# Optimization experiments

Hardware: AMD Instinct MI355X
Metric: run time of the kernel (lower is better)

The kernel has to match this reference:

```python
import jax, jax.numpy as jnp
import numpy as np

# ---- config (matches init_kwargs + VMamba/MambaIR SS2D defaults) ----
B, LEN, C, H, W = 2, 3, 64, 64, 64
N_STATE = 16           # d_state
D_INNER = 2 * C        # expand=2
DT_RANK = C // 16      # ceil(d_model/16)
K = 4                  # 4 scan directions
EPS = 1e-5


def _ln_last(x, g, b):
    m = x.mean(-1, keepdims=True)
    v = x.var(-1, keepdims=True)
    return (x - m) * jax.lax.rsqrt(v + EPS) * g + b


def _instance_ln(x):
    # kalman.utils.layer_norm: normalize each sample over (C,H,W), no affine
    m = x.mean(axis=(1, 2, 3), keepdims=True)
    v = x.var(axis=(1, 2, 3), keepdims=True)
    return (x - m) * jax.lax.rsqrt(v + EPS)


def _gn(x, g, b):
    # GroupNorm with num_groups=1 on NCHW
    m = x.mean(axis=(1, 2, 3), keepdims=True)
    v = x.var(axis=(1, 2, 3), keepdims=True)
    return (x - m) * jax.lax.rsqrt(v + EPS) * g[None, :, None, None] + b[None, :, None, None]


def _conv2d(x, w, b, groups=1):
    y = jax.lax.conv_general_dilated(x, w, (1, 1), 'SAME',
            dimension_numbers=('NCHW', 'OIHW', 'NCHW'), feature_group_count=groups)
    return y + b[None, :, None, None]


def _selective_scan(xs, dts, Bs, Cs, A, Ds, dt_bias):
    # xs, dts: (Bt,K,D,L); Bs, Cs: (Bt,K,N,L); A: (K,D,N); Ds, dt_bias: (K,D)
    delta = jax.nn.softplus(dts + dt_bias[None, :, :, None])
    u_t = jnp.moveaxis(xs, -1, 0)      # (L,Bt,K,D)
    d_t = jnp.moveaxis(delta, -1, 0)
    B_t = jnp.moveaxis(Bs, -1, 0)      # (L,Bt,K,N)
    C_t = jnp.moveaxis(Cs, -1, 0)
    h0 = jnp.zeros((xs.shape[0], K, xs.shape[2], A.shape[-1]), xs.dtype)

    def step(h, inp):
        u, d, Bv, Cv = inp
        dA = jnp.exp(d[..., None] * A)                                  # (Bt,K,D,N)
        h = dA * h + d[..., None] * Bv[:, :, None, :] * u[..., None]
        y = jnp.einsum('bkdn,bkn->bkd', h, Cv)
        return h, y

    _, ys = jax.lax.scan(step, h0, (u_t, d_t, B_t, C_t))
    ys = jnp.moveaxis(ys, 0, -1)                                        # (Bt,K,D,L)
    return ys + xs * Ds[None, :, :, None]


def _ss2d(x, in_proj_w, dwconv_w, dwconv_b, x_proj_w, dt_proj_w, dt_proj_b,
          A_logs, Ds, out_norm_g, out_norm_b, out_proj_w):
    Bt, Hh, Ww, Cc = x.shape
    L = Hh * Ww
    xz = x @ in_proj_w.T                               # (Bt,H,W,2*Di)
    xx, z = jnp.split(xz, 2, axis=-1)
    xx = jnp.transpose(xx, (0, 3, 1, 2))               # (Bt,Di,H,W)
    xx = jax.nn.silu(_conv2d(xx, dwconv_w, dwconv_b, groups=D_INNER))
    hw = xx.reshape(Bt, D_INNER, L)
    wh = jnp.transpose(xx, (0, 1, 3, 2)).reshape(Bt, D_INNER, L)
    xs = jnp.stack([hw, wh, hw[..., ::-1], wh[..., ::-1]], axis=1)      # (Bt,4,Di,L)
    x_dbl = jnp.einsum('bkdl,kcd->bkcl', xs, x_proj_w)
    dts = jnp.einsum('bkrl,kdr->bkdl', x_dbl[:, :, :DT_RANK], dt_proj_w)
    Bs = x_dbl[:, :, DT_RANK:DT_RANK + N_STATE]
    Cs = x_dbl[:, :, DT_RANK + N_STATE:]
    A = -jnp.exp(A_logs)                               # (K,Di,N)
    out_y = _selective_scan(xs, dts, Bs, Cs, A, Ds, dt_proj_b)
    inv = out_y[:, 2:4, :, ::-1]

    def wh2hw(y):
        return jnp.transpose(y.reshape(Bt, D_INNER, Ww, Hh), (0, 1, 3, 2)).reshape(Bt, D_INNER, L)

    y = out_y[:, 0] + inv[:, 0] + wh2hw(out_y[:, 1]) + wh2hw(inv[:, 1])
    y = jnp.transpose(y.reshape(Bt, D_INNER, Hh, Ww), (0, 2, 3, 1))
    y = _ln_last(y, out_norm_g, out_norm_b)
    y = y * jax.nn.silu(z)
    return y @ out_proj_w.T


def setup_inputs() -> dict:
    key = jax.random.key(0)
    ks = jax.random.split(key, 16)
    rn = lambda k, s, sc=0.05: jax.random.normal(k, s, jnp.float32) * sc
    inp = {}
    inp['image_sequence'] = jax.random.normal(ks[0], (B, LEN, C, H, W), jnp.float32)
    inp['difficult_zone'] = jax.random.normal(ks[1], (B, C, H, W), jnp.float32)
    inp['sigma'] = jax.random.uniform(ks[2], (B, C, H, W), jnp.float32)
    inp['gn1_g'] = jnp.ones((3 * C,)); inp['gn1_b'] = jnp.zeros((3 * C,))
    inp['conv1_w'] = rn(ks[3], (C, 3 * C, 3, 3)); inp['conv1_b'] = jnp.zeros((C,))
    inp['gn2_g'] = jnp.ones((C,)); inp['gn2_b'] = jnp.zeros((C,))
    inp['conv2_w'] = rn(ks[4], (C, C, 3, 3)); inp['conv2_b'] = jnp.zeros((C,))
    inp['skip_w'] = rn(ks[5], (C, 3 * C, 1, 1)); inp['skip_b'] = jnp.zeros((C,))
    inp['ln1_g'] = jnp.ones((C,)); inp['ln1_b'] = jnp.zeros((C,))
    inp['ln2_g'] = jnp.ones((C,)); inp['ln2_b'] = jnp.zeros((C,))
    inp['in_proj_w'] = rn(ks[6], (2 * D_INNER, C))
    inp['dwconv_w'] = rn(ks[7], (D_INNER, 1, 3, 3)); inp['dwconv_b'] = jnp.zeros((D_INNER,))
    inp['x_proj_w'] = rn(ks[8], (K, DT_RANK + 2 * N_STATE, D_INNER))
    inp['dt_proj_w'] = rn(ks[9], (K, D_INNER, DT_RANK), 0.2)
    inp['dt_proj_b'] = rn(ks[10], (K, D_INNER), 0.1)
    inp['A_logs'] = jnp.log(jnp.broadcast_to(jnp.arange(1, N_STATE + 1, dtype=jnp.float32), (K, D_INNER, N_STATE)))
    inp['Ds'] = jnp.ones((K, D_INNER))
    inp['out_norm_g'] = jnp.ones((D_INNER,)); inp['out_norm_b'] = jnp.zeros((D_INNER,))
    inp['out_proj_w'] = rn(ks[11], (C, D_INNER))
    inp['fc1_w'] = rn(ks[12], (C, C)); inp['fc1_b'] = jnp.zeros((C,))
    inp['fc2_w'] = rn(ks[13], (C, C)); inp['fc2_b'] = jnp.zeros((C,))
    return inp


def reference(image_sequence, difficult_zone, sigma,
              gn1_g, gn1_b, conv1_w, conv1_b, gn2_g, gn2_b, conv2_w, conv2_b, skip_w, skip_b,
              ln1_g, ln1_b, ln2_g, ln2_b,
              in_proj_w, dwconv_w, dwconv_b, x_proj_w, dt_proj_w, dt_proj_b,
              A_logs, Ds, out_norm_g, out_norm_b, out_proj_w,
              fc1_w, fc1_b, fc2_w, fc2_b):
    Bsz, Lf, Cc, Hh, Ww = image_sequence.shape
    # per-frame layer_norm; frames are independent so fold them into batch
    img = _instance_ln(image_sequence.reshape(Bsz * Lf, Cc, Hh, Ww)).reshape(Bsz, Lf, Cc, Hh, Ww)
    dz = jnp.broadcast_to(difficult_zone[:, None], (Bsz, Lf, Cc, Hh, Ww))
    sg = jnp.broadcast_to(sigma[:, None], (Bsz, Lf, Cc, Hh, Ww))
    x = jnp.concatenate([dz, img, sg], axis=2).reshape(Bsz * Lf, 3 * Cc, Hh, Ww)
    # ConvolutionalResBlock (GN -> SiLU -> conv, x2, + 1x1 skip)
    h = _conv2d(jax.nn.silu(_gn(x, gn1_g, gn1_b)), conv1_w, conv1_b)
    h = _conv2d(jax.nn.silu(_gn(h, gn2_g, gn2_b)), conv2_w, conv2_b)
    x = h + _conv2d(x, skip_w, skip_b)
    # VSSBlock (pre-norm): x + SS2D(LN(x)); x + Mlp(LN(x))
    x = jnp.transpose(x, (0, 2, 3, 1))                 # NHWC
    x = x + _ss2d(_ln_last(x, ln1_g, ln1_b), in_proj_w, dwconv_w, dwconv_b,
                  x_proj_w, dt_proj_w, dt_proj_b, A_logs, Ds,
                  out_norm_g, out_norm_b, out_proj_w)
    xm = _ln_last(x, ln2_g, ln2_b)
    x = x + (jax.nn.gelu(xm @ fc1_w.T + fc1_b) @ fc2_w.T + fc2_b)
    x = jnp.transpose(x, (0, 3, 1, 2)).reshape(Bsz, Lf, Cc, Hh, Ww)
    return x
```

## Files before the change

kernel.cpp:

```cpp
#include <hip/hip_runtime.h>
#include <hip/hip_bf16.h>

typedef unsigned short ushortT;
typedef short short8v __attribute__((ext_vector_type(8)));
typedef float float4v __attribute__((ext_vector_type(4)));

#define NBL 6
#define NC 64
#define NC3 192
#define NHW 4096
#define NDI 128
#define NNS 16
#define NDR 4
#define NK 4
#define NL 4096
#define NCH 128
#define SCLEN 32
#define NSTATE 49152
#define NSAMP 262144

static const size_t F_XCAT  = 0;
static const size_t F_ACT1  = 4718592;
static const size_t F_H1    = 9437184;
static const size_t F_ACT2  = 11010048;
static const size_t F_H2    = 12582912;
static const size_t F_XRES  = 14155776;
static const size_t F_XXIN  = 15728640;
static const size_t F_Z     = 18874368;
static const size_t F_XXC   = 22020096;
static const size_t F_XDBL  = 25165824;
static const size_t F_YS    = 28704768;
static const size_t F_WTS   = 41287680;
static const size_t F_X1    = 44433408;
static const size_t F_X2    = 46006272;
static const size_t F_STATS = 47579136;
static const size_t F_TOTAL = 47579184;

__device__ __forceinline__ float wred64(float v) {
#pragma unroll
  for (int m = 32; m; m >>= 1) v += __shfl_xor(v, m, 64);
  return v;
}

__device__ __forceinline__ float silu(float v) {
  return v / (1.f + __expf(-v));
}

__device__ __forceinline__ ushortT f2bf(float f) {
  unsigned int u = __builtin_bit_cast(unsigned int, f);
  unsigned int r = (u + 0x7FFFu + ((u >> 16) & 1u)) >> 16;
  return (ushortT)r;
}

__device__ __forceinline__ float bf2f(ushortT u) {
  return __builtin_bit_cast(float, (unsigned int)u << 16);
}

__device__ __forceinline__ int map_pos(int k, int l) {
  if (k == 0) return l;
  if (k == 1) return ((l & 63) << 6) | (l >> 6);
  if (k == 2) return 4095 - l;
  int lp = 4095 - l;
  return ((lp & 63) << 6) | (lp >> 6);
}

__device__ __forceinline__ float softplus_fast(float a) {
  float t = exp2f(a * 1.44269504f);
  float r = 0.69314718f * __log2f(1.f + t);
  return (a > 20.f) ? a : r;
}

__device__ __forceinline__ void pow_tree(float E1, float4v& e0, float4v& e1,
                                         float4v& e2, float4v& e3) {
  float E2 = E1 * E1, E3 = E2 * E1, E4 = E2 * E2;
  float E5 = E4 * E1, E6 = E4 * E2, E7 = E4 * E3, E8 = E4 * E4;
  e0[0] = E1; e0[1] = E2; e0[2] = E3; e0[3] = E4;
  e1[0] = E5; e1[1] = E6; e1[2] = E7; e1[3] = E8;
  e2[0] = E8 * E1; e2[1] = E8 * E2; e2[2] = E8 * E3; e2[3] = E8 * E4;
  e3[0] = E8 * E5; e3[1] = E8 * E6; e3[2] = E8 * E7; e3[3] = E8 * E8;
}

__global__ __launch_bounds__(256) void prep_kernel(const float* __restrict__ skw,
                                                   const float* __restrict__ ipw,
                                                   const float* __restrict__ opw,
                                                   const float* __restrict__ f1w,
                                                   const float* __restrict__ f2w,
                                                   const float* __restrict__ c1w,
                                                   const float* __restrict__ c2w,
                                                   float* __restrict__ wt_sk,
                                                   float* __restrict__ wt_ip,
                                                   float* __restrict__ wt_op,
                                                   float* __restrict__ wt_f1,
                                                   float* __restrict__ wt_f2,
                                                   ushortT* __restrict__ wb1,
                                                   ushortT* __restrict__ wb2) {
  int bi = blockIdx.x;
  int t = threadIdx.x;
  if (bi < 48) {
    int id = bi * 256 + t;
    int c = id / 64, o = id % 64;
    wt_sk[id] = skw[o * 192 + c];
  } else if (bi < 112) {
    int id = (bi - 48) * 256 + t;
    int c = id / 256, o = id % 256;
    wt_ip[id] = ipw[o * 64 + c];
  } else if (bi < 144) {
    int id = (bi - 112) * 256 + t;
    int c = id / 64, o = id % 64;
    wt_op[id] = opw[o * 128 + c];
  } else if (bi < 160) {
    int id = (bi - 144) * 256 + t;
    int c = id / 64, o = id % 64;
    wt_f1[id] = f1w[o * 64 + c];
  } else if (bi < 176) {
    int id = (bi - 160) * 256 + t;
    int c = id / 64, o = id % 64;
    wt_f2[id] = f2w[o * 64 + c];
  } else if (bi < 608) {
    int id = (bi - 176) * 256 + t;
    int j = id & 7, lane = (id >> 3) & 63, nt = (id >> 9) & 3;
    int rest = id >> 11;
    int kt = rest % 6, tap = rest / 6;
    int oc = nt * 16 + (lane & 15);
    int ic = kt * 32 + ((lane >> 4) << 3) + j;
    int r = tap / 3, s = tap % 3;
    wb1[id] = f2bf(c1w[(((size_t)oc * 192 + ic) * 3 + r) * 3 + s]);
  } else {
    int id = (bi - 608) * 256 + t;
    int j = id & 7, lane = (id >> 3) & 63, nt = (id >> 9) & 3;
    int rest = id >> 11;
    int kt = rest % 2, tap = rest / 2;
    int oc = nt * 16 + (lane & 15);
    int ic = kt * 32 + ((lane >> 4) << 3) + j;
    int r = tap / 3, s = tap % 3;
    wb2[id] = f2bf(c2w[(((size_t)oc * 64 + ic) * 3 + r) * 3 + s]);
  }
}

__global__ __launch_bounds__(256) void stats1_all_kernel(const float* __restrict__ img,
                                                         const float* __restrict__ dz,
                                                         const float* __restrict__ sg,
                                                         double* __restrict__ part) {
  int bi = blockIdx.x;
  int s = bi >> 5, j = bi & 31;
  const float* srcb = (s < 6) ? (img + (size_t)s * NSAMP)
                   : (s < 8) ? (dz + (size_t)(s - 6) * NSAMP)
                             : (sg + (size_t)(s - 8) * NSAMP);
  int slice = NSAMP >> 5;
  const float4* p = (const float4*)(srcb + (size_t)j * slice);
  int n4 = slice >> 2;
  double dsum = 0.0, dsq = 0.0;
  for (int i = threadIdx.x; i < n4; i += 256) {
    float4 v = p[i];
    dsum += (double)((v.x + v.y) + (v.z + v.w));
    dsq += (double)v.x * v.x + (double)v.y * v.y + (double)v.z * v.z + (double)v.w * v.w;
  }
  __shared__ double s1[256], s2[256];
  s1[threadIdx.x] = dsum; s2[threadIdx.x] = dsq;
  __syncthreads();
  for (int off = 128; off; off >>= 1) {
    if (threadIdx.x < off) { s1[threadIdx.x] += s1[threadIdx.x + off]; s2[threadIdx.x] += s2[threadIdx.x + off]; }
    __syncthreads();
  }
  if (threadIdx.x == 0) { part[2 * bi] = s1[0]; part[2 * bi + 1] = s2[0]; }
}

__global__ __launch_bounds__(256) void stats1_kernel(const float* __restrict__ in, int n,
                                                     double* __restrict__ part) {
  int bi = blockIdx.x;
  int s = bi >> 5, j = bi & 31;
  int slice = n >> 5;
  const float4* p = (const float4*)(in + (size_t)s * n + (size_t)j * slice);
  int n4 = slice >> 2;
  double dsum = 0.0, dsq = 0.0;
  for (int i = threadIdx.x; i < n4; i += 256) {
    float4 v = p[i];
    dsum += (double)((v.x + v.y) + (v.z + v.w));
    dsq += (double)v.x * v.x + (double)v.y * v.y + (double)v.z * v.z + (double)v.w * v.w;
  }
  __shared__ double s1[256], s2[256];
  s1[threadIdx.x] = dsum; s2[threadIdx.x] = dsq;
  __syncthreads();
  for (int off = 128; off; off >>= 1) {
    if (threadIdx.x < off) { s1[threadIdx.x] += s1[threadIdx.x + off]; s2[threadIdx.x] += s2[threadIdx.x + off]; }
    __syncthreads();
  }
  if (threadIdx.x == 0) { part[2 * bi] = s1[0]; part[2 * bi + 1] = s2[0]; }
}

__global__ __launch_bounds__(64) void stats2_kernel(const double* __restrict__ part, int n,
                                                    float* __restrict__ mean_out,
                                                    float* __restrict__ rstd_out) {
  int s = blockIdx.x;
  int lane = threadIdx.x;
  double sum = 0.0, sq = 0.0;
  if (lane < 32) { sum = part[2 * (s * 32 + lane)]; sq = part[2 * (s * 32 + lane) + 1]; }
#pragma unroll
  for (int m = 16; m; m >>= 1) { sum += __shfl_xor(sum, m, 64); sq += __shfl_xor(sq, m, 64); }
  if (lane == 0) {
    double mean = sum / n;
    double var = sq / n - mean * mean;
    mean_out[s] = (float)mean;
    rstd_out[s] = (float)(1.0 / sqrt(var + 1e-5));
  }
}

__global__ __launch_bounds__(64) void stats2_comb_kernel(const double* __restrict__ part,
                                                         float* __restrict__ stats) {
  int s = blockIdx.x;
  int lane = threadIdx.x;
  if (s < 6) {
    double sum = 0.0, sq = 0.0;
    if (lane < 32) { sum = part[2 * (s * 32 + lane)]; sq = part[2 * (s * 32 + lane) + 1]; }
#pragma unroll
    for (int m = 16; m; m >>= 1) { sum += __shfl_xor(sum, m, 64); sq += __shfl_xor(sq, m, 64); }
    if (lane == 0) {
      double mean = sum / NSAMP;
      double var = sq / NSAMP - mean * mean;
      stats[s] = (float)mean;
      stats[8 + s] = (float)(1.0 / sqrt(var + 1e-5));
    }
    return;
  }
  if (lane == 0) {
    double sums[10], sqs[10];
    for (int q = 0; q < 10; ++q) {
      double a = 0.0, b2 = 0.0;
      for (int j = 0; j < 32; ++j) { a += part[2 * (q * 32 + j)]; b2 += part[2 * (q * 32 + j) + 1]; }
      sums[q] = a; sqs[q] = b2;
    }
    const double N = (double)NSAMP;
    for (int bl = 0; bl < 6; ++bl) {
      int b = bl / 3;
      double mi = sums[bl] / N;
      double vi = sqs[bl] / N - mi * mi;
      double ssq_norm = N * (vi / (vi + 1e-5));
      double sum_cat = sums[6 + b] + sums[8 + b];
      double ssq_cat = sqs[6 + b] + ssq_norm + sqs[8 + b];
      double mean = sum_cat / (3.0 * N);
      double var = ssq_cat / (3.0 * N) - mean * mean;
      stats[16 + bl] = (float)mean;
      stats[24 + bl] = (float)(1.0 / sqrt(var + 1e-5));
    }
  }
}

__global__ __launch_bounds__(256) void gnsilu_cat_kernel(const float* __restrict__ img,
                                                         const float* __restrict__ dz,
                                                         const float* __restrict__ sg,
                                                         const float* __restrict__ g,
                                                         const float* __restrict__ b,
                                                         const float* __restrict__ stats,
                                                         ushortT* __restrict__ outb) {
  int bi = blockIdx.x;
  int bl = bi >> 6, h = bi & 63;
  int bb = bl / 3;
  __shared__ ushortT tile[NC3][66];
  float mi = stats[bl], rsi = stats[8 + bl];
  float mc = stats[16 + bl], rsc = stats[24 + bl];
  int t = threadIdx.x;
  for (int idx = t; idx < NC3 * 64; idx += 256) {
    int ch = idx >> 6, w = idx & 63;
    int hw = (h << 6) + w;
    float v;
    if (ch < 64) v = dz[((size_t)bb * NC + ch) * NHW + hw];
    else if (ch < 128) v = (img[((size_t)bl * NC + (ch - 64)) * NHW + hw] - mi) * rsi;
    else v = sg[((size_t)bb * NC + (ch - 128)) * NHW + hw];
    v = (v - mc) * rsc * g[ch] + b[ch];
    tile[ch][w] = f2bf(silu(v));
  }
  __syncthreads();
  constexpr int C8 = NC3 / 8;
  for (int idx = t; idx < 64 * C8; idx += 256) {
    int w = idx / C8, c8 = idx % C8;
    short8v v;
#pragma unroll
    for (int j = 0; j < 8; ++j) v[j] = (short)tile[c8 * 8 + j][w];
    *(short8v*)&outb[(size_t)(bl * 4096 + h * 64 + w) * NC3 + c8 * 8] = v;
  }
}

__global__ __launch_bounds__(256) void gnsilu_t_kernel(const float* __restrict__ in,
                                                       const float* __restrict__ g,
                                                       const float* __restrict__ b,
                                                       const float* __restrict__ stats,
                                                       ushortT* __restrict__ outb) {
  int bi = blockIdx.x;
  int bl = bi >> 6, h = bi & 63;
  __shared__ ushortT tile[NC][66];
  float m = stats[bl], rs = stats[8 + bl];
  int t = threadIdx.x;
  for (int idx = t; idx < NC * 64; idx += 256) {
    int ch = idx >> 6, w = idx & 63;
    float v = in[(((size_t)bl * NC + ch) << 12) + (h << 6) + w];
    v = (v - m) * rs * g[ch] + b[ch];
    tile[ch][w] = f2bf(silu(v));
  }
  __syncthreads();
  constexpr int C8 = NC / 8;
  for (int idx = t; idx < 64 * C8; idx += 256) {
    int w = idx / C8, c8 = idx % C8;
    short8v v;
#pragma unroll
    for (int j = 0; j < 8; ++j) v[j] = (short)tile[c8 * 8 + j][w];
    *(short8v*)&outb[(size_t)(bl * 4096 + h * 64 + w) * NC + c8 * 8] = v;
  }
}

template <int CIN>
__global__ __launch_bounds__(256) void conv_mfma_kernel(const ushortT* __restrict__ actb,
                                                        const ushortT* __restrict__ wb,
                                                        const float* __restrict__ bias,
                                                        float* __restrict__ out) {
  constexpr int KT = CIN / 32;
  constexpr int STRIDE = CIN + 8;
  constexpr int C8 = CIN / 8;
  int bi = blockIdx.x;
  int nh = bi & 1;
  int h = (bi >> 1) & 63;
  int bl = bi >> 7;
  int t = threadIdx.x;
  int wv = t >> 6, lane = t & 63;
  __shared__ ushortT lds[66 * STRIDE];
  float4v acc0 = {0.f, 0.f, 0.f, 0.f};
  float4v acc1 = {0.f, 0.f, 0.f, 0.f};
  int lrow = lane & 15;
  int lk = (lane >> 4) << 3;
  for (int dy = 0; dy < 3; ++dy) {
    int hh = h + dy - 1;
    bool valid = (hh >= 0) && (hh < 64);
    int hc = valid ? hh : 0;
    if (dy) __syncthreads();
    const ushortT* src = actb + (size_t)(bl * 4096 + hc * 64) * CIN;
    for (int idx = t; idx < 64 * C8; idx += 256) {
      int w = idx / C8, c8 = idx % C8;
      short8v v = {0, 0, 0, 0, 0, 0, 0, 0};
      if (valid) v = *(const short8v*)&src[(size_t)w * CIN + c8 * 8];
      *(short8v*)&lds[(w + 1) * STRIDE + c8 * 8] = v;
    }
    if (t < 2 * C8) {
      int which = t / C8, c8 = t % C8;
      short8v z = {0, 0, 0, 0, 0, 0, 0, 0};
      *(short8v*)&lds[(which ? 65 : 0) * STRIDE + c8 * 8] = z;
    }
    __syncthreads();
    for (int dx = 0; dx < 3; ++dx) {
      int tap = dy * 3 + dx;
      int wl = (wv << 4) + lrow + dx;
#pragma unroll
      for (int kt = 0; kt < KT; ++kt) {
        short8v a = *(const short8v*)&lds[wl * STRIDE + kt * 32 + lk];
        const ushortT* wp = wb + ((size_t)(((tap * KT + kt) * 4 + (nh << 1)) * 64 + lane) << 3);
        short8v b0 = *(const short8v*)&wp[0];
        short8v b1 = *(const short8v*)&wp[512];
        acc0 = __builtin_amdgcn_mfma_f32_16x16x32_bf16(a, b0, acc0, 0, 0, 0);
        acc1 = __builtin_amdgcn_mfma_f32_16x16x32_bf16(a, b1, acc1, 0, 0, 0);
      }
    }
  }
  int oc0 = (nh << 5) + lrow;
  int oc1 = oc0 + 16;
  int w0 = (wv << 4) + ((lane >> 4) << 2);
  float bv0 = bias[oc0], bv1 = bias[oc1];
  float4 o0 = make_float4(acc0[0] + bv0, acc0[1] + bv0, acc0[2] + bv0, acc0[3] + bv0);
  float4 o1 = make_float4(acc1[0] + bv1, acc1[1] + bv1, acc1[2] + bv1, acc1[3] + bv1);
  *(float4*)&out[(((size_t)bl * 64 + oc0) << 12) + (h << 6) + w0] = o0;
  *(float4*)&out[(((size_t)bl * 64 + oc1) << 12) + (h << 6) + w0] = o1;
}

__global__ __launch_bounds__(256) void skip_kernel(const float* __restrict__ img,
                                                   const float* __restrict__ dz,
                                                   const float* __restrict__ sg,
                                                   const float* __restrict__ stats,
                                                   const float* __restrict__ h2,
                                                   const float* __restrict__ skwt,
                                                   const float* __restrict__ skb,
                                                   float* __restrict__ xres) {
  int bi = blockIdx.x;
  int bl = bi >> 6, h = bi & 63;
  int bb = bl / 3;
  int t = threadIdx.x;
  int oc = t & 63, w0 = (t >> 6) << 4;
  float mi = stats[bl], rsi = stats[8 + bl];
  __shared__ float lds[64][64];
  float acc[16];
#pragma unroll
  for (int i = 0; i < 16; ++i) acc[i] = 0.f;
  for (int cc = 0; cc < 3; ++cc) {
    __syncthreads();
    for (int idx = t; idx < 4096; idx += 256) {
      int ch = idx >> 6, w = idx & 63;
      int hw = (h << 6) + w;
      float v;
      if (cc == 0) v = dz[((size_t)bb * NC + ch) * NHW + hw];
      else if (cc == 1) v = (img[((size_t)bl * NC + ch) * NHW + hw] - mi) * rsi;
      else v = sg[((size_t)bb * NC + ch) * NHW + hw];
      lds[ch][w] = v;
    }
    __syncthreads();
    for (int ch = 0; ch < 64; ++ch) {
      float wv = skwt[((cc << 6) + ch) * 64 + oc];
#pragma unroll
      for (int i = 0; i < 16; ++i) acc[i] += wv * lds[ch][w0 + i];
    }
  }
  float bv = skb[oc];
  int p0 = (h << 6) + w0;
#pragma unroll
  for (int i = 0; i < 16; ++i) {
    float hv = h2[(((size_t)bl * 64 + oc) << 12) + p0 + i];
    xres[((size_t)bl * NHW + p0 + i) * 64 + oc] = acc[i] + bv + hv;
  }
}

__global__ __launch_bounds__(256) void inproj_kernel(const float* __restrict__ xres,
                                                     const float* __restrict__ g,
                                                     const float* __restrict__ b,
                                                     const float* __restrict__ wt,
                                                     float* __restrict__ xxin,
                                                     float* __restrict__ z) {
  int wv = threadIdx.x >> 6, lane = threadIdx.x & 63;
  size_t pi0 = (size_t)blockIdx.x << 4;
  __shared__ float xb[64][16];
  float gv = g[lane], bv = b[lane];
#pragma unroll
  for (int j = 0; j < 4; ++j) {
    int p = (wv << 2) + j;
    float x = xres[(pi0 + p) * 64 + lane];
    float s = wred64(x);
    float s2 = wred64(x * x);
    float m = s * (1.f / 64), var = s2 * (1.f / 64) - m * m;
    float rstd = rsqrtf(var + 1e-5f);
    xb[lane][p] = (x - m) * rstd * gv + bv;
  }
  __syncthreads();
  int oc = (wv << 6) + lane;
  float4v a0 = {0.f, 0.f, 0.f, 0.f}, a1 = a0, a2 = a0, a3 = a0;
  for (int c = 0; c < 64; ++c) {
    float w = wt[(c << 8) + oc];
    const float4v* xr = (const float4v*)&xb[c][0];
    a0 += w * xr[0];
    a1 += w * xr[1];
    a2 += w * xr[2];
    a3 += w * xr[3];
  }
  float acc[16];
  *(float4v*)&acc[0] = a0;
  *(float4v*)&acc[4] = a1;
  *(float4v*)&acc[8] = a2;
  *(float4v*)&acc[12] = a3;
  float* dst = (oc < 128) ? xxin : z;
  int oco = (oc < 128) ? oc : (oc - 128);
#pragma unroll
  for (int p = 0; p < 16; ++p) dst[((pi0 + p) << 7) + oco] = acc[p];
}

__global__ __launch_bounds__(256) void dwconv_kernel(const float* __restrict__ xx,
                                                     const float* __restrict__ w,
                                                     const float* __restrict__ b,
                                                     float* __restrict__ out) {
  size_t gid = (size_t)blockIdx.x * 256 + threadIdx.x;
  int d = gid & 127;
  size_t pi = gid >> 7;
  int p = (int)(pi & 4095);
  int bl = (int)(pi >> 12);
  int h = p >> 6, wq = p & 63;
  float acc = b[d];
  const float* wr = w + d * 9;
#pragma unroll
  for (int dy = -1; dy <= 1; ++dy) {
    int hh = h + dy;
    if (hh < 0 || hh >= 64) continue;
#pragma unroll
    for (int dx = -1; dx <= 1; ++dx) {
      int ww = wq + dx;
      if (ww < 0 || ww >= 64) continue;
      acc += wr[(dy + 1) * 3 + (dx + 1)] * xx[(((size_t)bl << 12) + (hh << 6) + ww) * 128 + d];
    }
  }
  out[pi * 128 + d] = silu(acc);
}

__global__ __launch_bounds__(256) void xdbl_kernel(const float* __restrict__ xxc,
                                                   const float* __restrict__ xpw,
                                                   float* __restrict__ xdbl) {
  int bi = blockIdx.x;
  int lt = bi & 63;
  int korder = (bi >> 6) & 1;
  int bl = bi >> 7;
  int lbase = lt << 6;
  __shared__ float xs[64 * 128];
  int t = threadIdx.x;
#pragma unroll
  for (int it = 0; it < 8; ++it) {
    int idx = it * 256 + t;
    int i = idx >> 5, d4 = idx & 31;
    int l = lbase + i;
    int pos = korder ? (((l & 63) << 6) | (l >> 6)) : l;
    float4 v = *(const float4*)&xxc[((size_t)bl * NHW + pos) * 128 + (d4 << 2)];
    int slot = d4 ^ (i & 7);
    *(float4*)&xs[i * 128 + (slot << 2)] = v;
  }
  __syncthreads();
  int wv = __builtin_amdgcn_readfirstlane(t >> 6);
  int lane = t & 63;
  int k_w = korder + ((wv >= 2) ? 2 : 0);
  int c0 = (wv & 1) * 18;
  float acc[18];
#pragma unroll
  for (int j = 0; j < 18; ++j) acc[j] = 0.f;
  const float* wbase = xpw + (size_t)(k_w * 36 + c0) * 128;
  for (int d4 = 0; d4 < 32; ++d4) {
    int slot = d4 ^ (lane & 7);
    float4 x4 = *(const float4*)&xs[lane * 128 + (slot << 2)];
#pragma unroll
    for (int j = 0; j < 18; ++j) {
      float4 w4 = *(const float4*)&wbase[j * 128 + (d4 << 2)];
      acc[j] += w4.x * x4.x + w4.y * x4.y + w4.z * x4.z + w4.w * x4.w;
    }
  }
  int lout = (k_w < 2) ? (lbase + lane) : (4095 - lbase - lane);
  size_t obase = ((size_t)(bl * 4 + k_w) * 36 + c0) * (size_t)NL + lout;
#pragma unroll
  for (int j = 0; j < 18; ++j)
    xdbl[obase + (size_t)j * NL] = acc[j];
}

__global__ __launch_bounds__(128) void scan_pass1_kernel(const float* __restrict__ xdbl,
                                                         const float* __restrict__ xxc,
                                                         const float* __restrict__ dtw,
                                                         const float* __restrict__ dtb,
                                                         const float* __restrict__ Alog,
                                                         float* __restrict__ chunkSdt,
                                                         ushortT* __restrict__ chunkH16) {
  int bi = blockIdx.x;
  int chunk = bi & (NCH - 1);
  int bk = bi >> 7;
  int k = bk & 3, bl = bk >> 2;
  int d = threadIdx.x;
  float4 wv = *(const float4*)(dtw + (size_t)(((k << 7) + d) << 2));
  float bias = dtb[(k << 7) + d];
  const float* ar = Alog + (size_t)(((k << 7) + d) << 4);
  float a1v = -__expf(ar[0]) * 1.44269504f;
  bool geom = true;
#pragma unroll
  for (int n = 1; n < 16; ++n) {
    float an = -__expf(ar[n]) * 1.44269504f;
    geom = geom && (fabsf(an - (float)(n + 1) * a1v) <= 1e-3f * fabsf((float)(n + 1) * a1v) + 1e-6f);
  }
  __shared__ float xd[SCLEN][20];
  int l0 = chunk << 5;
  for (int idx = threadIdx.x; idx < 20 * SCLEN; idx += 128) {
    int c = idx >> 5, li = idx & 31;
    xd[li][c] = xdbl[((size_t)bk * 36 + c) * (size_t)NL + l0 + li];
  }
  __syncthreads();
  const float* uB = xxc + ((size_t)bl << 19) + d;
  float4v h0 = {0.f, 0.f, 0.f, 0.f}, h1 = h0, h2 = h0, h3 = h0;
  float sdt = 0.f;
  float u_nxt = uB[(size_t)map_pos(k, l0) << 7];
  if (geom) {
#pragma unroll 2
    for (int li = 0; li < SCLEN; ++li) {
      float u = u_nxt;
      int nl = (li < SCLEN - 1) ? (li + 1) : (SCLEN - 1);
      u_nxt = uB[(size_t)map_pos(k, l0 + nl) << 7];
      const float4v* row = (const float4v*)&xd[li][0];
      float4v q0 = row[0];
      float accq = bias + wv.x * q0[0] + wv.y * q0[1] + wv.z * q0[2] + wv.w * q0[3];
      float dt = softplus_fast(accq);
      float dtu = dt * u;
      sdt += dt;
      float4v b0 = row[1], b1 = row[2], b2 = row[3], b3 = row[4];
      float4v e0, e1, e2, e3;
      pow_tree(exp2f(a1v * dt), e0, e1, e2, e3);
      h0 = e0 * h0 + dtu * b0;
      h1 = e1 * h1 + dtu * b1;
      h2 = e2 * h2 + dtu * b2;
      h3 = e3 * h3 + dtu * b3;
    }
  } else {
    float4v a0v, a1q, a2q, a3q;
#pragma unroll
    for (int j = 0; j < 4; ++j) {
      a0v[j] = -__expf(ar[j]) * 1.44269504f;
      a1q[j] = -__expf(ar[4 + j]) * 1.44269504f;
      a2q[j] = -__expf(ar[8 + j]) * 1.44269504f;
      a3q[j] = -__expf(ar[12 + j]) * 1.44269504f;
    }
    for (int li = 0; li < SCLEN; ++li) {
      float u = u_nxt;
      int nl = (li < SCLEN - 1) ? (li + 1) : (SCLEN - 1);
      u_nxt = uB[(size_t)map_pos(k, l0 + nl) << 7];
      const float4v* row = (const float4v*)&xd[li][0];
      float4v q0 = row[0];
      float accq = bias + wv.x * q0[0] + wv.y * q0[1] + wv.z * q0[2] + wv.w * q0[3];
      float dt = softplus_fast(accq);
      float dtu = dt * u;
      sdt += dt;
      float4v b0 = row[1], b1 = row[2], b2 = row[3], b3 = row[4];
      float4v e0, e1, e2, e3;
#pragma unroll
      for (int j = 0; j < 4; ++j) {
        e0[j] = exp2f(a0v[j] * dt);
        e1[j] = exp2f(a1q[j] * dt);
        e2[j] = exp2f(a2q[j] * dt);
        e3[j] = exp2f(a3q[j] * dt);
      }
      h0 = e0 * h0 + dtu * b0;
      h1 = e1 * h1 + dtu * b1;
      h2 = e2 * h2 + dtu * b2;
      h3 = e3 * h3 + dtu * b3;
    }
  }
  size_t base = (size_t)chunk * NSTATE + (((size_t)bk << 7) + (size_t)d) * 16;
  chunkSdt[(size_t)chunk * 3072 + (bk << 7) + d] = sdt;
  short8v s0, s1;
#pragma unroll
  for (int j = 0; j < 4; ++j) {
    s0[j] = (short)f2bf(h0[j]);
    s0[4 + j] = (short)f2bf(h1[j]);
    s1[j] = (short)f2bf(h2[j]);
    s1[4 + j] = (short)f2bf(h3[j]);
  }
  *(short8v*)&chunkH16[base + 0] = s0;
  *(short8v*)&chunkH16[base + 8] = s1;
}

__global__ __launch_bounds__(256) void scan_pass2_kernel(const float* __restrict__ chunkSdt,
                                                         const ushortT* __restrict__ chunkH16,
                                                         const float* __restrict__ Alog,
                                                         ushortT* __restrict__ chunkHS16) {
  size_t state = (size_t)blockIdx.x * 256 + threadIdx.x;
  float an = -__expf(Alog[state & 8191]) * 1.44269504f;
  int kd = (int)(state >> 4);
  float h = 0.f;
  for (int j = 0; j < NCH; ++j) {
    size_t idx = (size_t)j * NSTATE + state;
    chunkHS16[idx] = f2bf(h);
    float sdt = chunkSdt[(size_t)j * 3072 + kd];
    h = exp2f(an * sdt) * h + bf2f(chunkH16[idx]);
  }
}

__global__ __launch_bounds__(128) void scan_pass3_kernel(const float* __restrict__ xdbl,
                                                         const float* __restrict__ xxc,
                                                         const float* __restrict__ dtw,
                                                         const float* __restrict__ dtb,
                                                         const float* __restrict__ Alog,
                                                         const ushortT* __restrict__ chunkHS16,
                                                         ushortT* __restrict__ ys16) {
  int bi = blockIdx.x;
  int chunk = bi & (NCH - 1);
  int bk = bi >> 7;
  int k = bk & 3, bl = bk >> 2;
  int d = threadIdx.x;
  float4 wv = *(const float4*)(dtw + (size_t)(((k << 7) + d) << 2));
  float bias = dtb[(k << 7) + d];
  const float* ar = Alog + (size_t)(((k << 7) + d) << 4);
  float a1v = -__expf(ar[0]) * 1.44269504f;
  bool geom = true;
#pragma unroll
  for (int n = 1; n < 16; ++n) {
    float an = -__expf(ar[n]) * 1.44269504f;
    geom = geom && (fabsf(an - (float)(n + 1) * a1v) <= 1e-3f * fabsf((float)(n + 1) * a1v) + 1e-6f);
  }
  __shared__ float xd[SCLEN][40];
  int l0 = chunk << 5;
  for (int idx = threadIdx.x; idx < 36 * SCLEN; idx += 128) {
    int c = idx >> 5, li = idx & 31;
    xd[li][c] = xdbl[((size_t)bk * 36 + c) * (size_t)NL + l0 + li];
  }
  __syncthreads();
  const float* uB = xxc + ((size_t)bl << 19) + d;
  ushortT* yB = ys16 + ((size_t)bk << 19) + d;
  size_t base = (size_t)chunk * NSTATE + (((size_t)bk << 7) + (size_t)d) * 16;
  float4v h0, h1, h2, h3;
  {
    short8v s0 = *(const short8v*)&chunkHS16[base + 0];
    short8v s1 = *(const short8v*)&chunkHS16[base + 8];
#pragma unroll
    for (int j = 0; j < 4; ++j) {
      h0[j] = bf2f((ushortT)s0[j]);
      h1[j] = bf2f((ushortT)s0[4 + j]);
      h2[j] = bf2f((ushortT)s1[j]);
      h3[j] = bf2f((ushortT)s1[4 + j]);
    }
  }
  float u_nxt = uB[(size_t)map_pos(k, l0) << 7];
  if (geom) {
#pragma unroll 2
    for (int li = 0; li < SCLEN; ++li) {
      float u = u_nxt;
      int nl = (li < SCLEN - 1) ? (li + 1) : (SCLEN - 1);
      u_nxt = uB[(size_t)map_pos(k, l0 + nl) << 7];
      const float4v* row = (const float4v*)&xd[li][0];
      float4v q0 = row[0];
      float accq = bias + wv.x * q0[0] + wv.y * q0[1] + wv.z * q0[2] + wv.w * q0[3];
      float dt = softplus_fast(accq);
      float dtu = dt * u;
      float4v b0 = row[1], b1 = row[2], b2 = row[3], b3 = row[4];
      float4v c0 = row[5], c1 = row[6], c2 = row[7], c3 = row[8];
      float4v e0, e1, e2, e3;
      pow_tree(exp2f(a1v * dt), e0, e1, e2, e3);
      h0 = e0 * h0 + dtu * b0;
      h1 = e1 * h1 + dtu * b1;
      h2 = e2 * h2 + dtu * b2;
      h3 = e3 * h3 + dtu * b3;
      float4v sy = h0 * c0;
      sy += h1 * c1;
      sy += h2 * c2;
      sy += h3 * c3;
      yB[(size_t)(l0 + li) << 7] = f2bf((sy[0] + sy[1]) + (sy[2] + sy[3]));
    }
  } else {
    float4v a0v, a1q, a2q, a3q;
#pragma unroll
    for (int j = 0; j < 4; ++j) {
      a0v[j] = -__expf(ar[j]) * 1.44269504f;
      a1q[j] = -__expf(ar[4 + j]) * 1.44269504f;
      a2q[j] = -__expf(ar[8 + j]) * 1.44269504f;
      a3q[j] = -__expf(ar[12 + j]) * 1.44269504f;
    }
    for (int li = 0; li < SCLEN; ++li) {
      float u = u_nxt;
      int nl = (li < SCLEN - 1) ? (li + 1) : (SCLEN - 1);
      u_nxt = uB[(size_t)map_pos(k, l0 + nl) << 7];
      const float4v* row = (const float4v*)&xd[li][0];
      float4v q0 = row[0];
      float accq = bias + wv.x * q0[0] + wv.y * q0[1] + wv.z * q0[2] + wv.w * q0[3];
      float dt = softplus_fast(accq);
      float dtu = dt * u;
      float4v b0 = row[1], b1 = row[2], b2 = row[3], b3 = row[4];
      float4v c0 = row[5], c1 = row[6], c2 = row[7], c3 = row[8];
      float4v e0, e1, e2, e3;
#pragma unroll
      for (int j = 0; j < 4; ++j) {
        e0[j] = exp2f(a0v[j] * dt);
        e1[j] = exp2f(a1q[j] * dt);
        e2[j] = exp2f(a2q[j] * dt);
        e3[j] = exp2f(a3q[j] * dt);
      }
      h0 = e0 * h0 + dtu * b0;
      h1 = e1 * h1 + dtu * b1;
      h2 = e2 * h2 + dtu * b2;
      h3 = e3 * h3 + dtu * b3;
      float4v sy = h0 * c0;
      sy += h1 * c1;
      sy += h2 * c2;
      sy += h3 * c3;
      yB[(size_t)(l0 + li) << 7] = f2bf((sy[0] + sy[1]) + (sy[2] + sy[3]));
    }
  }
}

__global__ __launch_bounds__(256) void outproj_kernel(const ushortT* __restrict__ ys16,
                                                      const float* __restrict__ xxc,
                                                      const float* __restrict__ Ds,
                                                      const float* __restrict__ z,
                                                      const float* __restrict__ ong,
                                                      const float* __restrict__ onb,
                                                      const float* __restrict__ opwt,
                                                      const float* __restrict__ xres,
                                                      float* __restrict__ x1) {
  int wv = threadIdx.x >> 6, lane = threadIdx.x & 63;
  size_t pi0 = (size_t)blockIdx.x << 4;
  __shared__ float gb[128][16];
  float og0 = ong[lane], ob0 = onb[lane];
  float og1 = ong[64 + lane], ob1 = onb[64 + lane];
  float ds0 = Ds[lane] + Ds[128 + lane] + Ds[256 + lane] + Ds[384 + lane];
  float ds1 = Ds[64 + lane] + Ds[192 + lane] + Ds[320 + lane] + Ds[448 + lane];
#pragma unroll
  for (int j = 0; j < 4; ++j) {
    int p = (wv << 2) + j;
    size_t pp = pi0 + p;
    int bl = (int)(pp >> 12);
    int pg = (int)(pp & 4095);
    int h = pg >> 6, w = pg & 63;
    int l1 = (w << 6) | h;
    size_t base = ((size_t)bl * 4) << 12;
    size_t i0 = (base + pg) << 7;
    size_t i1 = (base + 4096 + l1) << 7;
    size_t i2 = (base + 2 * 4096 + (4095 - pg)) << 7;
    size_t i3 = (base + 3 * 4096 + (4095 - l1)) << 7;
    float xx0 = xxc[(pp << 7) + lane], xx1 = xxc[(pp << 7) + 64 + lane];
    float y0 = bf2f(ys16[i0 + lane]) + bf2f(ys16[i1 + lane]) + bf2f(ys16[i2 + lane]) +
               bf2f(ys16[i3 + lane]) + xx0 * ds0;
    float y1 = bf2f(ys16[i0 + 64 + lane]) + bf2f(ys16[i1 + 64 + lane]) +
               bf2f(ys16[i2 + 64 + lane]) + bf2f(ys16[i3 + 64 + lane]) + xx1 * ds1;
    float s = wred64(y0 + y1);
    float s2 = wred64(y0 * y0 + y1 * y1);
    float m = s * (1.f / 128), var = s2 * (1.f / 128) - m * m;
    float rstd = rsqrtf(var + 1e-5f);
    float z0 = z[(pp << 7) + lane], z1 = z[(pp << 7) + 64 + lane];
    gb[lane][p] = ((y0 - m) * rstd * og0 + ob0) * silu(z0);
    gb[64 + lane][p] = ((y1 - m) * rstd * og1 + ob1) * silu(z1);
  }
  __syncthreads();
  int p0 = wv << 2;
  float4v acc = {0.f, 0.f, 0.f, 0.f};
  for (int c = 0; c < 128; ++c) {
    float w = opwt[(c << 6) + lane];
    acc += w * (*(const float4v*)&gb[c][p0]);
  }
  float accs[4];
  *(float4v*)&accs[0] = acc;
#pragma unroll
  for (int j = 0; j < 4; ++j) {
    size_t pp = pi0 + p0 + j;
    x1[pp * 64 + lane] = xres[pp * 64 + lane] + accs[j];
  }
}

__global__ __launch_bounds__(256) void mlp_kernel(const float* __restrict__ x1,
                                                  const float* __restrict__ g2,
                                                  const float* __restrict__ b2,
                                                  const float* __restrict__ w1t,
                                                  const float* __restrict__ bb1,
                                                  const float* __restrict__ w2t,
                                                  const float* __restrict__ bb2,
                                                  float* __restrict__ out) {
  int wv = threadIdx.x >> 6, lane = threadIdx.x & 63;
  size_t pi0 = (size_t)blockIdx.x << 4;
  __shared__ float xb[64][16], tb[64][16];
  __shared__ float ot[64][17];
  float gv = g2[lane], bv = b2[lane];
  float xsave[4];
#pragma unroll
  for (int j = 0; j < 4; ++j) {
    int p = (wv << 2) + j;
    float xv = x1[(pi0 + p) * 64 + lane];
    xsave[j] = xv;
    float s = wred64(xv), s2 = wred64(xv * xv);
    float m = s * (1.f / 64), var = s2 * (1.f / 64) - m * m;
    float rstd = rsqrtf(var + 1e-5f);
    xb[lane][p] = (xv - m) * rstd * gv + bv;
  }
  __syncthreads();
  int p0 = wv << 2;
  float bb1v = bb1[lane];
  float4v acc = {bb1v, bb1v, bb1v, bb1v};
  for (int c = 0; c < 64; ++c) {
    float w = w1t[(c << 6) + lane];
    acc += w * (*(const float4v*)&xb[c][p0]);
  }
  float us[4];
  *(float4v*)&us[0] = acc;
#pragma unroll
  for (int j = 0; j < 4; ++j) {
    float u = us[j];
    float tt = tanhf(0.7978845608028654f * (u + 0.044715f * u * u * u));
    tb[lane][p0 + j] = 0.5f * u * (1.f + tt);
  }
  __syncthreads();
  float bb2v = bb2[lane];
  float4v acc2 = {bb2v, bb2v, bb2v, bb2v};
  for (int c = 0; c < 64; ++c) {
    float w = w2t[(c << 6) + lane];
    acc2 += w * (*(const float4v*)&tb[c][p0]);
  }
  float o2[4];
  *(float4v*)&o2[0] = acc2;
#pragma unroll
  for (int j = 0; j < 4; ++j)
    ot[lane][p0 + j] = xsave[j] + o2[j];
  __syncthreads();
  int bl = (int)(pi0 >> 12);
  int pg0 = (int)(pi0 & 4095);
  int t = threadIdx.x;
  int c = t >> 2, q = t & 3;
  float4 v = make_float4(ot[c][(q << 2) + 0], ot[c][(q << 2) + 1],
                         ot[c][(q << 2) + 2], ot[c][(q << 2) + 3]);
  *(float4*)&out[(((size_t)bl * 64 + c) << 12) + pg0 + (q << 2)] = v;
}

extern "C" void kernel_launch(void* const* d_in, const int* in_sizes, int n_in,
                              void* d_out, int out_size, void* d_ws, size_t ws_size,
                              hipStream_t stream) {
  const float* img  = (const float*)d_in[0];
  const float* dz   = (const float*)d_in[1];
  const float* sg   = (const float*)d_in[2];
  const float* gn1g = (const float*)d_in[3];
  const float* gn1b = (const float*)d_in[4];
  const float* c1w  = (const float*)d_in[5];
  const float* c1b  = (const float*)d_in[6];
  const float* gn2g = (const float*)d_in[7];
  const float* gn2b = (const float*)d_in[8];
  const float* c2w  = (const float*)d_in[9];
  const float* c2b  = (const float*)d_in[10];
  const float* skw  = (const float*)d_in[11];
  const float* skb  = (const float*)d_in[12];
  const float* ln1g = (const float*)d_in[13];
  const float* ln1b = (const float*)d_in[14];
  const float* ln2g = (const float*)d_in[15];
  const float* ln2b = (const float*)d_in[16];
  const float* ipw  = (const float*)d_in[17];
  const float* dww  = (const float*)d_in[18];
  const float* dwb  = (const float*)d_in[19];
  const float* xpw  = (const float*)d_in[20];
  const float* dtw  = (const float*)d_in[21];
  const float* dtb  = (const float*)d_in[22];
  const float* Alog = (const float*)d_in[23];
  const float* Dsp  = (const float*)d_in[24];
  const float* ong  = (const float*)d_in[25];
  const float* onb  = (const float*)d_in[26];
  const float* opw  = (const float*)d_in[27];
  const float* f1w  = (const float*)d_in[28];
  const float* f1b  = (const float*)d_in[29];
  const float* f2w  = (const float*)d_in[30];
  const float* f2b  = (const float*)d_in[31];

  float* out = (float*)d_out;
  float* ws = (float*)d_ws;
  if (ws_size < F_TOTAL * sizeof(float)) return;

  float* h1    = ws + F_H1;
  float* h2    = ws + F_H2;
  float* xres  = ws + F_XRES;
  float* xxin  = ws + F_XXIN;
  float* zbuf  = ws + F_Z;
  float* xxc   = ws + F_XXC;
  float* xdbl  = ws + F_XDBL;
  float* x1    = ws + F_X1;
  float* stats = ws + F_STATS;
  ushortT* act1b = (ushortT*)(ws + F_ACT1);
  ushortT* act2b = (ushortT*)(ws + F_ACT2);
  double* part  = (double*)(ws + F_X2);
  float* wt_sk = ws + F_WTS;
  float* wt_ip = ws + F_WTS + 16384;
  float* wt_op = ws + F_WTS + 32768;
  float* wt_f1 = ws + F_WTS + 40960;
  float* wt_f2 = ws + F_WTS + 45056;
  ushortT* wb1 = (ushortT*)(ws + F_WTS + 49152);
  ushortT* wb2 = wb1 + 110592;
  ushortT* ys16     = (ushortT*)(ws + F_YS);
  ushortT* chunkH16 = (ushortT*)(ws + F_YS + 6291456);
  float*   chunkSdt = ws + F_YS + 6291456 + 3145728;
  ushortT* chunkHS16 = (ushortT*)(ws + F_XCAT);

  prep_kernel<<<752, 256, 0, stream>>>(skw, ipw, opw, f1w, f2w, c1w, c2w,
                                       wt_sk, wt_ip, wt_op, wt_f1, wt_f2, wb1, wb2);
  stats1_all_kernel<<<320, 256, 0, stream>>>(img, dz, sg, part);
  stats2_comb_kernel<<<7, 64, 0, stream>>>(part, stats);
  gnsilu_cat_kernel<<<NBL * 64, 256, 0, stream>>>(img, dz, sg, gn1g, gn1b, stats, act1b);
  conv_mfma_kernel<NC3><<<NBL * 64 * 2, 256, 0, stream>>>(act1b, wb1, c1b, h1);
  stats1_kernel<<<NBL * 32, 256, 0, stream>>>(h1, NC * NHW, part);
  stats2_kernel<<<NBL, 64, 0, stream>>>(part, NC * NHW, stats + 32, stats + 40);
  gnsilu_t_kernel<<<NBL * 64, 256, 0, stream>>>(h1, gn2g, gn2b, stats + 32, act2b);
  conv_mfma_kernel<NC><<<NBL * 64 * 2, 256, 0, stream>>>(act2b, wb2, c2b, h2);
  skip_kernel<<<NBL * 64, 256, 0, stream>>>(img, dz, sg, stats, h2, wt_sk, skb, xres);
  inproj_kernel<<<1536, 256, 0, stream>>>(xres, ln1g, ln1b, wt_ip, xxin, zbuf);
  dwconv_kernel<<<12288, 256, 0, stream>>>(xxin, dww, dwb, xxc);
  xdbl_kernel<<<NBL * 2 * 64, 256, 0, stream>>>(xxc, xpw, xdbl);
  scan_pass1_kernel<<<24 * NCH, 128, 0, stream>>>(xdbl, xxc, dtw, dtb, Alog, chunkSdt, chunkH16);
  scan_pass2_kernel<<<192, 256, 0, stream>>>(chunkSdt, chunkH16, Alog, chunkHS16);
  scan_pass3_kernel<<<24 * NCH, 128, 0, stream>>>(xdbl, xxc, dtw, dtb, Alog, chunkHS16, ys16);
  outproj_kernel<<<1536, 256, 0, stream>>>(ys16, xxc, Dsp, zbuf, ong, onb, wt_op, xres, x1);
  mlp_kernel<<<1536, 256, 0, stream>>>(x1, ln2g, ln2b, wt_f1, f1b, wt_f2, f2b, out);
}
```

Baseline: 324.2 us.

## Precompute scan A parameters in prep, pack two chunks per block, vectorize pass2

```diff
diff --git a/kernel.cpp b/kernel.cpp
--- a/kernel.cpp
+++ b/kernel.cpp
@@ -3,15 +3,13 @@
 
 typedef unsigned short ushortT;
 typedef short short8v __attribute__((ext_vector_type(8)));
+typedef short short4v __attribute__((ext_vector_type(4)));
 typedef float float4v __attribute__((ext_vector_type(4)));
 
 #define NBL 6
 #define NC 64
 #define NC3 192
 #define NHW 4096
-#define NDI 128
-#define NNS 16
-#define NDR 4
 #define NK 4
 #define NL 4096
 #define NCH 128
@@ -87,13 +85,15 @@
                                                    const float* __restrict__ f2w,
                                                    const float* __restrict__ c1w,
                                                    const float* __restrict__ c2w,
+                                                   const float* __restrict__ Alog,
                                                    float* __restrict__ wt_sk,
                                                    float* __restrict__ wt_ip,
                                                    float* __restrict__ wt_op,
                                                    float* __restrict__ wt_f1,
                                                    float* __restrict__ wt_f2,
                                                    ushortT* __restrict__ wb1,
-                                                   ushortT* __restrict__ wb2) {
+                                                   ushortT* __restrict__ wb2,
+                                                   float* __restrict__ aParam) {
   int bi = blockIdx.x;
   int t = threadIdx.x;
   if (bi < 48) {
@@ -125,7 +125,7 @@
     int ic = kt * 32 + ((lane >> 4) << 3) + j;
     int r = tap / 3, s = tap % 3;
     wb1[id] = f2bf(c1w[(((size_t)oc * 192 + ic) * 3 + r) * 3 + s]);
-  } else {
+  } else if (bi < 752) {
     int id = (bi - 608) * 256 + t;
     int j = id & 7, lane = (id >> 3) & 63, nt = (id >> 9) & 3;
     int rest = id >> 11;
@@ -134,6 +134,18 @@
     int ic = kt * 32 + ((lane >> 4) << 3) + j;
     int r = tap / 3, s = tap % 3;
     wb2[id] = f2bf(c2w[(((size_t)oc * 64 + ic) * 3 + r) * 3 + s]);
+  } else {
+    int kd = (bi - 752) * 256 + t;
+    const float* ar = Alog + (size_t)kd * 16;
+    float a1v = -__expf(ar[0]) * 1.44269504f;
+    bool geom = true;
+#pragma unroll
+    for (int n = 1; n < 16; ++n) {
+      float an = -__expf(ar[n]) * 1.44269504f;
+      geom = geom && (fabsf(an - (float)(n + 1) * a1v) <= 1e-3f * fabsf((float)(n + 1) * a1v) + 1e-6f);
+    }
+    aParam[kd] = a1v;
+    aParam[512 + kd] = geom ? 1.f : 0.f;
   }
 }
 
@@ -526,33 +538,30 @@
     xdbl[obase + (size_t)j * NL] = acc[j];
 }
 
-__global__ __launch_bounds__(128) void scan_pass1_kernel(const float* __restrict__ xdbl,
+__global__ __launch_bounds__(256) void scan_pass1_kernel(const float* __restrict__ xdbl,
                                                          const float* __restrict__ xxc,
                                                          const float* __restrict__ dtw,
                                                          const float* __restrict__ dtb,
                                                          const float* __restrict__ Alog,
+                                                         const float* __restrict__ aParam,
                                                          float* __restrict__ chunkSdt,
                                                          ushortT* __restrict__ chunkH16) {
   int bi = blockIdx.x;
-  int chunk = bi & (NCH - 1);
-  int bk = bi >> 7;
+  int half = threadIdx.x >> 7;
+  int d = threadIdx.x & 127;
+  int chunk = ((bi & 63) << 1) + half;
+  int bk = bi >> 6;
   int k = bk & 3, bl = bk >> 2;
-  int d = threadIdx.x;
   float4 wv = *(const float4*)(dtw + (size_t)(((k << 7) + d) << 2));
   float bias = dtb[(k << 7) + d];
-  const float* ar = Alog + (size_t)(((k << 7) + d) << 4);
-  float a1v = -__expf(ar[0]) * 1.44269504f;
-  bool geom = true;
-#pragma unroll
-  for (int n = 1; n < 16; ++n) {
-    float an = -__expf(ar[n]) * 1.44269504f;
-    geom = geom && (fabsf(an - (float)(n + 1) * a1v) <= 1e-3f * fabsf((float)(n + 1) * a1v) + 1e-6f);
-  }
-  __shared__ float xd[SCLEN][20];
+  int kd = (k << 7) + d;
+  float a1v = aParam[kd];
+  bool geom = aParam[512 + kd] > 0.5f;
+  __shared__ float xd[2][SCLEN][20];
   int l0 = chunk << 5;
-  for (int idx = threadIdx.x; idx < 20 * SCLEN; idx += 128) {
+  for (int idx = d; idx < 20 * SCLEN; idx += 128) {
     int c = idx >> 5, li = idx & 31;
-    xd[li][c] = xdbl[((size_t)bk * 36 + c) * (size_t)NL + l0 + li];
+    xd[half][li][c] = xdbl[((size_t)bk * 36 + c) * (size_t)NL + l0 + li];
   }
   __syncthreads();
   const float* uB = xxc + ((size_t)bl << 19) + d;
@@ -565,7 +574,7 @@
       float u = u_nxt;
       int nl = (li < SCLEN - 1) ? (li + 1) : (SCLEN - 1);
       u_nxt = uB[(size_t)map_pos(k, l0 + nl) << 7];
-      const float4v* row = (const float4v*)&xd[li][0];
+      const float4v* row = (const float4v*)&xd[half][li][0];
       float4v q0 = row[0];
       float accq = bias + wv.x * q0[0] + wv.y * q0[1] + wv.z * q0[2] + wv.w * q0[3];
       float dt = softplus_fast(accq);
@@ -580,6 +589,7 @@
       h3 = e3 * h3 + dtu * b3;
     }
   } else {
+    const float* ar = Alog + (size_t)kd * 16;
     float4v a0v, a1q, a2q, a3q;
 #pragma unroll
     for (int j = 0; j < 4; ++j) {
@@ -592,7 +602,7 @@
       float u = u_nxt;
       int nl = (li < SCLEN - 1) ? (li + 1) : (SCLEN - 1);
       u_nxt = uB[(size_t)map_pos(k, l0 + nl) << 7];
-      const float4v* row = (const float4v*)&xd[li][0];
+      const float4v* row = (const float4v*)&xd[half][li][0];
       float4v q0 = row[0];
       float accq = bias + wv.x * q0[0] + wv.y * q0[1] + wv.z * q0[2] + wv.w * q0[3];
       float dt = softplus_fast(accq);
@@ -631,45 +641,51 @@
                                                          const ushortT* __restrict__ chunkH16,
                                                          const float* __restrict__ Alog,
                                                          ushortT* __restrict__ chunkHS16) {
-  size_t state = (size_t)blockIdx.x * 256 + threadIdx.x;
-  float an = -__expf(Alog[state & 8191]) * 1.44269504f;
-  int kd = (int)(state >> 4);
-  float h = 0.f;
+  size_t s4 = ((size_t)blockIdx.x * 256 + threadIdx.x) * 4;
+  int kd = (int)(s4 >> 4);
+  int abase = (int)(s4 & 8191);
+  float4v an;
+#pragma unroll
+  for (int j = 0; j < 4; ++j) an[j] = -__expf(Alog[abase + j]) * 1.44269504f;
+  float4v h = {0.f, 0.f, 0.f, 0.f};
   for (int j = 0; j < NCH; ++j) {
-    size_t idx = (size_t)j * NSTATE + state;
-    chunkHS16[idx] = f2bf(h);
+    size_t idx = (size_t)j * NSTATE + s4;
+    short4v hs;
+#pragma unroll
+    for (int q = 0; q < 4; ++q) hs[q] = (short)f2bf(h[q]);
+    *(short4v*)&chunkHS16[idx] = hs;
     float sdt = chunkSdt[(size_t)j * 3072 + kd];
-    h = exp2f(an * sdt) * h + bf2f(chunkH16[idx]);
-  }
-}
-
-__global__ __launch_bounds__(128) void scan_pass3_kernel(const float* __restrict__ xdbl,
+    short4v hv = *(const short4v*)&chunkH16[idx];
+#pragma unroll
+    for (int q = 0; q < 4; ++q)
+      h[q] = exp2f(an[q] * sdt) * h[q] + bf2f((ushortT)hv[q]);
+  }
+}
+
+__global__ __launch_bounds__(256) void scan_pass3_kernel(const float* __restrict__ xdbl,
                                                          const float* __restrict__ xxc,
                                                          const float* __restrict__ dtw,
                                                          const float* __restrict__ dtb,
                                                          const float* __restrict__ Alog,
+                                                         const float* __restrict__ aParam,
                                                          const ushortT* __restrict__ chunkHS16,
                                                          ushortT* __restrict__ ys16) {
   int bi = blockIdx.x;
-  int chunk = bi & (NCH - 1);
-  int bk = bi >> 7;
+  int half = threadIdx.x >> 7;
+  int d = threadIdx.x & 127;
+  int chunk = ((bi & 63) << 1) + half;
+  int bk = bi >> 6;
   int k = bk & 3, bl = bk >> 2;
-  int d = threadIdx.x;
   float4 wv = *(const float4*)(dtw + (size_t)(((k << 7) + d) << 2));
   float bias = dtb[(k << 7) + d];
-  const float* ar = Alog + (size_t)(((k << 7) + d) << 4);
-  float a1v = -__expf(ar[0]) * 1.44269504f;
-  bool geom = true;
-#pragma unroll
-  for (int n = 1; n < 16; ++n) {
-    float an = -__expf(ar[n]) * 1.44269504f;
-    geom = geom && (fabsf(an - (float)(n + 1) * a1v) <= 1e-3f * fabsf((float)(n + 1) * a1v) + 1e-6f);
-  }
-  __shared__ float xd[SCLEN][40];
+  int kd = (k << 7) + d;
+  float a1v = aParam[kd];
+  bool geom = aParam[512 + kd] > 0.5f;
+  __shared__ float xd[2][SCLEN][40];
   int l0 = chunk << 5;
-  for (int idx = threadIdx.x; idx < 36 * SCLEN; idx += 128) {
+  for (int idx = d; idx < 36 * SCLEN; idx += 128) {
     int c = idx >> 5, li = idx & 31;
-    xd[li][c] = xdbl[((size_t)bk * 36 + c) * (size_t)NL + l0 + li];
+    xd[half][li][c] = xdbl[((size_t)bk * 36 + c) * (size_t)NL + l0 + li];
   }
   __syncthreads();
   const float* uB = xxc + ((size_t)bl << 19) + d;
@@ -694,7 +710,7 @@
       float u = u_nxt;
       int nl = (li < SCLEN - 1) ? (li + 1) : (SCLEN - 1);
       u_nxt = uB[(size_t)map_pos(k, l0 + nl) << 7];
-      const float4v* row = (const float4v*)&xd[li][0];
+      const float4v* row = (const float4v*)&xd[half][li][0];
       float4v q0 = row[0];
       float accq = bias + wv.x * q0[0] + wv.y * q0[1] + wv.z * q0[2] + wv.w * q0[3];
       float dt = softplus_fast(accq);
@@ -714,6 +730,7 @@
       yB[(size_t)(l0 + li) << 7] = f2bf((sy[0] + sy[1]) + (sy[2] + sy[3]));
     }
   } else {
+    const float* ar = Alog + (size_t)kd * 16;
     float4v a0v, a1q, a2q, a3q;
 #pragma unroll
     for (int j = 0; j < 4; ++j) {
@@ -726,7 +743,7 @@
       float u = u_nxt;
       int nl = (li < SCLEN - 1) ? (li + 1) : (SCLEN - 1);
       u_nxt = uB[(size_t)map_pos(k, l0 + nl) << 7];
-      const float4v* row = (const float4v*)&xd[li][0];
+      const float4v* row = (const float4v*)&xd[half][li][0];
       float4v q0 = row[0];
       float accq = bias + wv.x * q0[0] + wv.y * q0[1] + wv.z * q0[2] + wv.w * q0[3];
       float dt = softplus_fast(accq);
@@ -933,13 +950,14 @@
   float* wt_f2 = ws + F_WTS + 45056;
   ushortT* wb1 = (ushortT*)(ws + F_WTS + 49152);
   ushortT* wb2 = wb1 + 110592;
+  float* aParam = ws + F_WTS + 49152 + 73728 + 1024;
   ushortT* ys16     = (ushortT*)(ws + F_YS);
   ushortT* chunkH16 = (ushortT*)(ws + F_YS + 6291456);
   float*   chunkSdt = ws + F_YS + 6291456 + 3145728;
   ushortT* chunkHS16 = (ushortT*)(ws + F_XCAT);
 
-  prep_kernel<<<752, 256, 0, stream>>>(skw, ipw, opw, f1w, f2w, c1w, c2w,
-                                       wt_sk, wt_ip, wt_op, wt_f1, wt_f2, wb1, wb2);
+  prep_kernel<<<754, 256, 0, stream>>>(skw, ipw, opw, f1w, f2w, c1w, c2w, Alog,
+                                       wt_sk, wt_ip, wt_op, wt_f1, wt_f2, wb1, wb2, aParam);
   stats1_all_kernel<<<320, 256, 0, stream>>>(img, dz, sg, part);
   stats2_comb_kernel<<<7, 64, 0, stream>>>(part, stats);
   gnsilu_cat_kernel<<<NBL * 64, 256, 0, stream>>>(img, dz, sg, gn1g, gn1b, stats, act1b);
@@ -952,9 +970,9 @@
   inproj_kernel<<<1536, 256, 0, stream>>>(xres, ln1g, ln1b, wt_ip, xxin, zbuf);
   dwconv_kernel<<<12288, 256, 0, stream>>>(xxin, dww, dwb, xxc);
   xdbl_kernel<<<NBL * 2 * 64, 256, 0, stream>>>(xxc, xpw, xdbl);
-  scan_pass1_kernel<<<24 * NCH, 128, 0, stream>>>(xdbl, xxc, dtw, dtb, Alog, chunkSdt, chunkH16);
-  scan_pass2_kernel<<<192, 256, 0, stream>>>(chunkSdt, chunkH16, Alog, chunkHS16);
-  scan_pass3_kernel<<<24 * NCH, 128, 0, stream>>>(xdbl, xxc, dtw, dtb, Alog, chunkHS16, ys16);
+  scan_pass1_kernel<<<24 * 64, 256, 0, stream>>>(xdbl, xxc, dtw, dtb, Alog, aParam, chunkSdt, chunkH16);
+  scan_pass2_kernel<<<48, 256, 0, stream>>>(chunkSdt, chunkH16, Alog, chunkHS16);
+  scan_pass3_kernel<<<24 * 64, 256, 0, stream>>>(xdbl, xxc, dtw, dtb, Alog, aParam, chunkHS16, ys16);
   outproj_kernel<<<1536, 256, 0, stream>>>(ys16, xxc, Dsp, zbuf, ong, onb, wt_op, xres, x1);
   mlp_kernel<<<1536, 256, 0, stream>>>(x1, ln2g, ln2b, wt_f1, f1b, wt_f2, f2b, out);
 }
```

After: 328.3 us. Within noise of the previous version (+1.3%).
